# Performance work log

Measured on AMD Instinct MI355X. Metric: run time of the kernel, lower is better.

The kernel has to match this reference:

```python
import jax, jax.numpy as jnp
import numpy as np

DIMS = 96
HEADS = 2
E = 2.66
HID = int(DIMS * E)  # 255
B, H, W = 2, 256, 256
EPS = 1e-5


def setup_inputs() -> dict:
    key = jax.random.key(0)
    ks = jax.random.split(key, 8)
    s = 0.02
    return {
        "x": jax.random.normal(ks[0], (B, H, W, DIMS), jnp.float32),
        "ln1_gamma": jnp.ones((DIMS,), jnp.float32),
        "ln1_beta": jnp.zeros((DIMS,), jnp.float32),
        "ln2_gamma": jnp.ones((DIMS,), jnp.float32),
        "ln2_beta": jnp.zeros((DIMS,), jnp.float32),
        "qkv_w": jax.random.normal(ks[1], (DIMS, 3 * DIMS), jnp.float32) * s,
        "qkv_dw": jax.random.normal(ks[2], (3, 3, 3 * DIMS), jnp.float32) * s,
        "temperature": jnp.ones((HEADS, 1, 1), jnp.float32),
        "attn_out_w": jax.random.normal(ks[3], (DIMS, DIMS), jnp.float32) * s,
        "ffn_in_w": jax.random.normal(ks[4], (DIMS, 2 * HID), jnp.float32) * s,
        "ffn_dw": jax.random.normal(ks[5], (3, 3, 2 * HID), jnp.float32) * s,
        "ffn_out_w": jax.random.normal(ks[6], (HID, DIMS), jnp.float32) * s,
    }


def _layernorm(x, gamma, beta):
    # tf.nn.moments over channel axis (biased variance), per-pixel LN
    mu = jnp.mean(x, axis=-1, keepdims=True)
    var = jnp.var(x, axis=-1, keepdims=True)
    return (x - mu) / jnp.sqrt(var + EPS) * gamma + beta


def _dwconv3x3(x, k):
    # x: [B,H,W,C]; k: [3,3,C] depthwise kernel, SAME padding, no bias
    c = x.shape[-1]
    return jax.lax.conv_general_dilated(
        x, k[:, :, None, :], (1, 1), 'SAME',
        dimension_numbers=('NHWC', 'HWIO', 'NHWC'), feature_group_count=c)


def reference(x, ln1_gamma, ln1_beta, ln2_gamma, ln2_beta, qkv_w, qkv_dw,
              temperature, attn_out_w, ffn_in_w, ffn_dw, ffn_out_w):
    b, h, w, c = x.shape
    ch = c // HEADS  # per-head channels

    # ---- transposed (channel) attention branch ----
    y = _layernorm(x, ln1_gamma, ln1_beta)
    qkv = _dwconv3x3(jnp.einsum('bhwc,cd->bhwd', y, qkv_w), qkv_dw)
    q, k, v = jnp.split(qkv, 3, axis=-1)

    def to_heads(t):  # [b,h,w,heads*ch] -> [b,heads,ch,hw]
        return t.reshape(b, h * w, HEADS, ch).transpose(0, 2, 3, 1)

    q, k, v = to_heads(q), to_heads(k), to_heads(v)
    q = q / jnp.linalg.norm(q, axis=-1, keepdims=True)  # L2 over spatial dim
    k = k / jnp.linalg.norm(k, axis=-1, keepdims=True)
    # small [b,heads,ch,ch] attention matrix
    attn = jax.nn.softmax(jnp.einsum('bncs,bnds->bncd', q, k) * temperature, axis=-1)
    o = jnp.einsum('bncd,bnds->bncs', attn, v)  # [b,heads,ch,hw]
    o = o.transpose(0, 3, 1, 2).reshape(b, h, w, c)
    x = x + jnp.einsum('bhwc,cd->bhwd', o, attn_out_w)

    # ---- gated depthwise-conv FFN branch ----
    y = _layernorm(x, ln2_gamma, ln2_beta)
    hdd = _dwconv3x3(jnp.einsum('bhwc,cd->bhwd', y, ffn_in_w), ffn_dw)
    x1, x2 = jnp.split(hdd, 2, axis=-1)
    gated = jax.nn.gelu(x1, approximate=False) * x2  # tf.nn.gelu default = exact
    x = x + jnp.einsum('bhwc,cd->bhwd', gated, ffn_out_w)
    return x
```

## Files before the change

### kernel.cpp

```cpp
#include <hip/hip_runtime.h>
#include <hip/hip_bf16.h>

typedef __hip_bfloat16 bf16;
typedef __attribute__((ext_vector_type(8))) short short8;
typedef __attribute__((ext_vector_type(4))) float floatx4;

#define NPIX  131072
#define BATCH 2
#define HH    256
#define WW    256
#define CDIM  96
#define C3    288
#define HEADS 2
#define CH    48
#define HIDN  255
#define HWSZ  65536
#define EPSV  1e-5f

__device__ __forceinline__ float b2f(bf16 v) { return __bfloat162float(v); }
__device__ __forceinline__ bf16  f2b(float v) { return __float2bfloat16(v); }
__device__ __forceinline__ short f2bs(float v) { bf16 h = __float2bfloat16(v); return *reinterpret_cast<short*>(&h); }
__device__ __forceinline__ float lo16(unsigned u) { return __uint_as_float(u << 16); }
__device__ __forceinline__ float hi16(unsigned u) { return __uint_as_float(u & 0xffff0000u); }
__device__ __forceinline__ unsigned packbf(float lo, float hi) {
  return ((unsigned)(unsigned short)f2bs(hi) << 16) | (unsigned)(unsigned short)f2bs(lo);
}

__device__ __forceinline__ float fast_gelu(float x) {
  float ax = fabsf(x) * 0.70710678118654752440f;
  float t  = 1.f / (1.f + 0.3275911f * ax);
  float p  = ((((1.061405429f * t - 1.453152027f) * t + 1.421413741f) * t
               - 0.284496736f) * t + 0.254829592f) * t;
  float er = 1.f - p * __expf(-ax * ax);
  er = copysignf(er, x);
  return 0.5f * x * (1.f + er);
}

__global__ __launch_bounds__(256) void prep_wt(
    const float* __restrict__ qkv_w, const float* __restrict__ ffn_in_w,
    const float* __restrict__ ffn_out_w, const float* __restrict__ ffn_dw,
    bf16* __restrict__ WQ, bf16* __restrict__ WF1, bf16* __restrict__ WF2,
    bf16* __restrict__ WO, float* __restrict__ WDW)
{
  int gid = blockIdx.x * 256 + threadIdx.x;
  if (gid < 27648) {
    int n = gid / 96, k = gid - n * 96;
    WQ[gid] = f2b(qkv_w[k * C3 + n]);
  } else if (gid < 27648 + 24576) {
    int g = gid - 27648;
    int n = g / 96, k = g - n * 96;
    WF1[g] = f2b(n < HIDN ? ffn_in_w[k * (2 * HIDN) + n] : 0.f);
  } else if (gid < 27648 + 49152) {
    int g = gid - 27648 - 24576;
    int n = g / 96, k = g - n * 96;
    WF2[g] = f2b(n < HIDN ? ffn_in_w[k * (2 * HIDN) + HIDN + n] : 0.f);
  } else if (gid < 101376) {
    int g = gid - 27648 - 49152;
    int n = g / 256, k = g - n * 256;
    WO[g] = f2b(k < HIDN ? ffn_out_w[k * CDIM + n] : 0.f);
  } else {
    int idx = gid - 101376;
    if (idx < 4608) {
      int c = idx & 511;
      float v = 0.f;
      if (c < 255)                 v = ffn_dw[(idx >> 9) * 510 + c];
      else if (c >= 256 && c < 511) v = ffn_dw[(idx >> 9) * 510 + (c - 1)];
      WDW[idx] = v;
    }
  }
}

template<int BM, int BN, int KT, bool ADD_RES, bool OUT_BF16>
__global__ __launch_bounds__(256, 2) void mfma_gemm(
    const bf16* __restrict__ A, int lda,
    const bf16* __restrict__ Wt,
    void* __restrict__ outp, int ldo,
    const float* __restrict__ res, int ldr)
{
  constexpr int NK  = KT / 32;
  constexpr int NCT = BN / 16;
  constexpr int RT  = BM / 64;
  const int tid  = threadIdx.x;
  const long bm  = (long)blockIdx.x * BM;
  const int lane = tid & 63;
  const int wv   = tid >> 6;
  const int m15  = lane & 15;
  const int quad = lane >> 4;

  short8 areg[RT][NK];
  #pragma unroll
  for (int rt = 0; rt < RT; ++rt) {
    const bf16* ap = A + (bm + wv * (BM / 4) + rt * 16 + m15) * lda + quad * 8;
    #pragma unroll
    for (int kk = 0; kk < NK; ++kk)
      areg[rt][kk] = *reinterpret_cast<const short8*>(ap + kk * 32);
  }

  floatx4 acc[RT][NCT];
  #pragma unroll
  for (int rt = 0; rt < RT; ++rt)
    #pragma unroll
    for (int ct = 0; ct < NCT; ++ct)
      acc[rt][ct] = (floatx4){0.f, 0.f, 0.f, 0.f};

  const bf16* wp = Wt + m15 * KT + quad * 8;
  #pragma unroll
  for (int kk = 0; kk < NK; ++kk)
    #pragma unroll
    for (int ct = 0; ct < NCT; ++ct) {
      short8 b = *reinterpret_cast<const short8*>(wp + ct * 16 * KT + kk * 32);
      #pragma unroll
      for (int rt = 0; rt < RT; ++rt)
        acc[rt][ct] = __builtin_amdgcn_mfma_f32_16x16x32_bf16(areg[rt][kk], b, acc[rt][ct], 0, 0, 0);
    }

  #pragma unroll
  for (int rt = 0; rt < RT; ++rt)
    #pragma unroll
    for (int ct = 0; ct < NCT; ++ct) {
      int col = ct * 16 + m15;
      #pragma unroll
      for (int r = 0; r < 4; ++r) {
        long row = bm + wv * (BM / 4) + rt * 16 + quad * 4 + r;
        float v = acc[rt][ct][r];
        if (ADD_RES) v += res[row * ldr + col];
        if (OUT_BF16) ((bf16*)outp)[row * ldo + col] = f2b(v);
        else          ((float*)outp)[row * ldo + col] = v;
      }
    }
}

__global__ __launch_bounds__(256, 2) void mfma_gemm_ffn(
    const bf16* __restrict__ A,
    const bf16* __restrict__ Wt1, const bf16* __restrict__ Wt2,
    bf16* __restrict__ out1, bf16* __restrict__ out2)
{
  const bf16* Wt  = blockIdx.z ? Wt2 : Wt1;
  bf16* outp      = blockIdx.z ? out2 : out1;
  const int tid  = threadIdx.x;
  const long bm  = (long)blockIdx.x * 128;
  const int lane = tid & 63;
  const int wv   = tid >> 6;
  const int m15  = lane & 15;
  const int quad = lane >> 4;

  short8 areg[2][3];
  #pragma unroll
  for (int rt = 0; rt < 2; ++rt) {
    const bf16* ap = A + (bm + wv * 32 + rt * 16 + m15) * CDIM + quad * 8;
    #pragma unroll
    for (int kk = 0; kk < 3; ++kk)
      areg[rt][kk] = *reinterpret_cast<const short8*>(ap + kk * 32);
  }

  floatx4 acc[2][16];
  #pragma unroll
  for (int rt = 0; rt < 2; ++rt)
    #pragma unroll
    for (int ct = 0; ct < 16; ++ct)
      acc[rt][ct] = (floatx4){0.f, 0.f, 0.f, 0.f};

  const bf16* wp = Wt + m15 * 96 + quad * 8;
  #pragma unroll
  for (int kk = 0; kk < 3; ++kk)
    #pragma unroll
    for (int ct = 0; ct < 16; ++ct) {
      short8 b = *reinterpret_cast<const short8*>(wp + ct * 16 * 96 + kk * 32);
      #pragma unroll
      for (int rt = 0; rt < 2; ++rt)
        acc[rt][ct] = __builtin_amdgcn_mfma_f32_16x16x32_bf16(areg[rt][kk], b, acc[rt][ct], 0, 0, 0);
    }

  #pragma unroll
  for (int rt = 0; rt < 2; ++rt)
    #pragma unroll
    for (int ct = 0; ct < 16; ++ct) {
      int col = ct * 16 + m15;
      #pragma unroll
      for (int r = 0; r < 4; ++r) {
        long row = bm + wv * 32 + rt * 16 + quad * 4 + r;
        outp[row * 256 + col] = f2b(acc[rt][ct][r]);
      }
    }
}

__global__ __launch_bounds__(256, 2) void mfma_gemm_lnA(
    const float* __restrict__ X, const float* __restrict__ gam, const float* __restrict__ bet,
    const bf16* __restrict__ Wt,
    bf16* __restrict__ outp)
{
  const int tid  = threadIdx.x;
  const long bm  = (long)blockIdx.x * 128;
  const int lane = tid & 63;
  const int wv   = tid >> 6;
  const int m15  = lane & 15;
  const int quad = lane >> 4;

  float xv[2][24];
  #pragma unroll
  for (int rt = 0; rt < 2; ++rt) {
    const float* xp = X + (bm + wv * 32 + rt * 16 + m15) * CDIM + quad * 8;
    #pragma unroll
    for (int kk = 0; kk < 3; ++kk) {
      float4 t0 = *reinterpret_cast<const float4*>(xp + kk * 32);
      float4 t1 = *reinterpret_cast<const float4*>(xp + kk * 32 + 4);
      xv[rt][kk * 8 + 0] = t0.x; xv[rt][kk * 8 + 1] = t0.y; xv[rt][kk * 8 + 2] = t0.z; xv[rt][kk * 8 + 3] = t0.w;
      xv[rt][kk * 8 + 4] = t1.x; xv[rt][kk * 8 + 5] = t1.y; xv[rt][kk * 8 + 6] = t1.z; xv[rt][kk * 8 + 7] = t1.w;
    }
  }
  float gv[24], bv[24];
  #pragma unroll
  for (int kk = 0; kk < 3; ++kk) {
    float4 g0 = *reinterpret_cast<const float4*>(gam + kk * 32 + quad * 8);
    float4 g1 = *reinterpret_cast<const float4*>(gam + kk * 32 + quad * 8 + 4);
    float4 b0 = *reinterpret_cast<const float4*>(bet + kk * 32 + quad * 8);
    float4 b1 = *reinterpret_cast<const float4*>(bet + kk * 32 + quad * 8 + 4);
    gv[kk * 8 + 0] = g0.x; gv[kk * 8 + 1] = g0.y; gv[kk * 8 + 2] = g0.z; gv[kk * 8 + 3] = g0.w;
    gv[kk * 8 + 4] = g1.x; gv[kk * 8 + 5] = g1.y; gv[kk * 8 + 6] = g1.z; gv[kk * 8 + 7] = g1.w;
    bv[kk * 8 + 0] = b0.x; bv[kk * 8 + 1] = b0.y; bv[kk * 8 + 2] = b0.z; bv[kk * 8 + 3] = b0.w;
    bv[kk * 8 + 4] = b1.x; bv[kk * 8 + 5] = b1.y; bv[kk * 8 + 6] = b1.z; bv[kk * 8 + 7] = b1.w;
  }

  short8 areg[2][3];
  #pragma unroll
  for (int rt = 0; rt < 2; ++rt) {
    float s = 0.f, sq = 0.f;
    #pragma unroll
    for (int e = 0; e < 24; ++e) { s += xv[rt][e]; sq += xv[rt][e] * xv[rt][e]; }
    s  += __shfl_xor(s, 16);  s  += __shfl_xor(s, 32);
    sq += __shfl_xor(sq, 16); sq += __shfl_xor(sq, 32);
    float mean = s * (1.f / 96.f);
    float var  = sq * (1.f / 96.f) - mean * mean;
    float rstd = rsqrtf(var + EPSV);
    #pragma unroll
    for (int kk = 0; kk < 3; ++kk)
      #pragma unroll
      for (int j = 0; j < 8; ++j)
        areg[rt][kk][j] = f2bs((xv[rt][kk * 8 + j] - mean) * rstd * gv[kk * 8 + j] + bv[kk * 8 + j]);
  }

  floatx4 acc[2][18];
  #pragma unroll
  for (int rt = 0; rt < 2; ++rt)
    #pragma unroll
    for (int ct = 0; ct < 18; ++ct)
      acc[rt][ct] = (floatx4){0.f, 0.f, 0.f, 0.f};

  const bf16* wp = Wt + m15 * 96 + quad * 8;
  #pragma unroll
  for (int kk = 0; kk < 3; ++kk)
    #pragma unroll
    for (int ct = 0; ct < 18; ++ct) {
      short8 b = *reinterpret_cast<const short8*>(wp + ct * 16 * 96 + kk * 32);
      #pragma unroll
      for (int rt = 0; rt < 2; ++rt)
        acc[rt][ct] = __builtin_amdgcn_mfma_f32_16x16x32_bf16(areg[rt][kk], b, acc[rt][ct], 0, 0, 0);
    }

  #pragma unroll
  for (int rt = 0; rt < 2; ++rt)
    #pragma unroll
    for (int ct = 0; ct < 18; ++ct) {
      int col = ct * 16 + m15;
      #pragma unroll
      for (int r = 0; r < 4; ++r) {
        long row = bm + wv * 32 + rt * 16 + quad * 4 + r;
        outp[row * C3 + col] = f2b(acc[rt][ct][r]);
      }
    }
}

__global__ __launch_bounds__(256, 2) void mfma_gemm_attn(
    const bf16* __restrict__ A, const bf16* __restrict__ Mt,
    const float* __restrict__ res, const float* __restrict__ gam, const float* __restrict__ bet,
    float* __restrict__ outp, bf16* __restrict__ y2)
{
  const int tid  = threadIdx.x;
  const long bm  = (long)blockIdx.x * 128;
  const int lane = tid & 63;
  const int wv   = tid >> 6;
  const int m15  = lane & 15;
  const int quad = lane >> 4;

  short8 areg[2][3];
  #pragma unroll
  for (int rt = 0; rt < 2; ++rt) {
    const bf16* ap = A + (bm + wv * 32 + rt * 16 + m15) * 96 + quad * 8;
    #pragma unroll
    for (int kk = 0; kk < 3; ++kk)
      areg[rt][kk] = *reinterpret_cast<const short8*>(ap + kk * 32);
  }

  floatx4 acc[2][6];
  #pragma unroll
  for (int rt = 0; rt < 2; ++rt)
    #pragma unroll
    for (int ct = 0; ct < 6; ++ct)
      acc[rt][ct] = (floatx4){0.f, 0.f, 0.f, 0.f};

  const bf16* mp = Mt + (bm >> 16) * (CDIM * CDIM) + m15 * 96 + quad * 8;
  #pragma unroll
  for (int kk = 0; kk < 3; ++kk)
    #pragma unroll
    for (int ct = 0; ct < 6; ++ct) {
      short8 b = *reinterpret_cast<const short8*>(mp + ct * 16 * 96 + kk * 32);
      #pragma unroll
      for (int rt = 0; rt < 2; ++rt)
        acc[rt][ct] = __builtin_amdgcn_mfma_f32_16x16x32_bf16(areg[rt][kk], b, acc[rt][ct], 0, 0, 0);
    }

  float gv[6], bv[6];
  #pragma unroll
  for (int ct = 0; ct < 6; ++ct) { gv[ct] = gam[ct * 16 + m15]; bv[ct] = bet[ct * 16 + m15]; }

  #pragma unroll
  for (int rt = 0; rt < 2; ++rt)
    #pragma unroll
    for (int r = 0; r < 4; ++r) {
      long row = bm + wv * 32 + rt * 16 + quad * 4 + r;
      float v[6];
      float s = 0.f, sq = 0.f;
      #pragma unroll
      for (int ct = 0; ct < 6; ++ct) {
        v[ct] = acc[rt][ct][r] + res[row * CDIM + ct * 16 + m15];
        s += v[ct]; sq += v[ct] * v[ct];
      }
      #pragma unroll
      for (int off = 8; off; off >>= 1) { s += __shfl_xor(s, off); sq += __shfl_xor(sq, off); }
      float mean = s * (1.f / 96.f);
      float var  = sq * (1.f / 96.f) - mean * mean;
      float rstd = rsqrtf(var + EPSV);
      #pragma unroll
      for (int ct = 0; ct < 6; ++ct) {
        int col = ct * 16 + m15;
        outp[row * CDIM + col] = v[ct];
        y2[row * CDIM + col] = f2b((v[ct] - mean) * rstd * gv[ct] + bv[ct]);
      }
    }
}

__global__ __launch_bounds__(384, 2) void dwconv_plane(
    const bf16* __restrict__ in,
    const float* __restrict__ kw,
    bf16* __restrict__ outbase)
{
  __shared__ uint4 sm[12][19 * 10];
  const int tid = threadIdx.x;
  const int tx0 = blockIdx.x * 16;
  const int ty0 = (blockIdx.y & 31) * 8;
  const int b   = blockIdx.y >> 5;
  const int pl  = blockIdx.z;
  const int c0  = pl * 96;
  const long bbase = (long)b * HWSZ;
  bf16* out = outbase + (size_t)pl * NPIX * 96;

  const int lane = tid & 63;
  const int wv   = tid >> 6;

  for (int f = lane; f < 180; f += 64) {
    int row = f / 18, px = f - row * 18;
    int y = ty0 + row - 1, xx = tx0 + px - 1;
    uint4 ua = make_uint4(0u, 0u, 0u, 0u), ub = ua;
    if ((unsigned)y < (unsigned)HH && (unsigned)xx < (unsigned)WW) {
      const bf16* p = in + (bbase + (long)y * WW + xx) * C3 + c0;
      ua = *reinterpret_cast<const uint4*>(p + wv * 8);
      ub = *reinterpret_cast<const uint4*>(p + (wv + 6) * 8);
    }
    sm[wv][row * 19 + px]     = ua;
    sm[wv + 6][row * 19 + px] = ub;
  }
  asm volatile("s_waitcnt lgkmcnt(0)" ::: "memory");
  __builtin_amdgcn_sched_barrier(0);

  const int x  = lane & 15;
  const int yg = lane >> 4;

  #pragma unroll 1
  for (int cgi = 0; cgi < 2; ++cgi) {
    const int cg = wv + cgi * 6;
    const int cbu = __builtin_amdgcn_readfirstlane(c0 + cg * 8);
    float wgt[9][8];
    #pragma unroll
    for (int t = 0; t < 9; ++t) {
      float4 w0 = *reinterpret_cast<const float4*>(kw + t * C3 + cbu);
      float4 w1 = *reinterpret_cast<const float4*>(kw + t * C3 + cbu + 4);
      wgt[t][0] = w0.x; wgt[t][1] = w0.y; wgt[t][2] = w0.z; wgt[t][3] = w0.w;
      wgt[t][4] = w1.x; wgt[t][5] = w1.y; wgt[t][6] = w1.z; wgt[t][7] = w1.w;
    }
    #pragma unroll
    for (int yy = 0; yy < 2; ++yy) {
      const int ry = yg * 2 + yy;
      float acc[8] = {0.f, 0.f, 0.f, 0.f, 0.f, 0.f, 0.f, 0.f};
      #pragma unroll
      for (int dy = 0; dy < 3; ++dy)
        #pragma unroll
        for (int dx = 0; dx < 3; ++dx) {
          uint4 u = sm[cg][(ry + dy) * 19 + x + dx];
          const float* wt = wgt[dy * 3 + dx];
          acc[0] += lo16(u.x) * wt[0]; acc[1] += hi16(u.x) * wt[1];
          acc[2] += lo16(u.y) * wt[2]; acc[3] += hi16(u.y) * wt[3];
          acc[4] += lo16(u.z) * wt[4]; acc[5] += hi16(u.z) * wt[5];
          acc[6] += lo16(u.w) * wt[6]; acc[7] += hi16(u.w) * wt[7];
        }
      bf16* op = out + (bbase + (long)(ty0 + ry) * WW + tx0 + x) * 96 + cg * 8;
      __align__(16) bf16 ov[8];
      #pragma unroll
      for (int j = 0; j < 8; ++j) ov[j] = f2b(acc[j]);
      *reinterpret_cast<uint4*>(op) = *reinterpret_cast<const uint4*>(ov);
    }
    __builtin_amdgcn_sched_barrier(0);
  }
}

__global__ __launch_bounds__(512, 2) void dwgate512(
    const bf16* __restrict__ t1, const bf16* __restrict__ t2,
    const float* __restrict__ wdw, bf16* __restrict__ out)
{
  __shared__ uint4 sm[8][19 * 10];
  const int tid = threadIdx.x;
  const int tx0 = blockIdx.x * 16;
  const int ty0 = (blockIdx.y & 31) * 8;
  const long bbase = (long)(blockIdx.y >> 5) * HWSZ;
  const int c0  = blockIdx.z * 64;

  const int lane = tid & 63;
  const int wv   = tid >> 6;
  const int cb   = c0 + wv * 8;
  const int cbu  = __builtin_amdgcn_readfirstlane(cb);

  uint4 t2r[3];
  #pragma unroll
  for (int i = 0; i < 3; ++i) {
    int f = lane + i * 64;
    int row = f / 18, px = f - row * 18;
    int y = ty0 + row - 1, xx = tx0 + px - 1;
    bool ok = (f < 180) && ((unsigned)y < (unsigned)HH) && ((unsigned)xx < (unsigned)WW);
    long base = (bbase + (long)y * WW + xx) * 256 + cb;
    uint4 u1 = make_uint4(0u, 0u, 0u, 0u);
    t2r[i]   = make_uint4(0u, 0u, 0u, 0u);
    if (ok) {
      u1     = *reinterpret_cast<const uint4*>(t1 + base);
      t2r[i] = *reinterpret_cast<const uint4*>(t2 + base);
    }
    if (f < 180) sm[wv][row * 19 + px] = u1;
  }
  asm volatile("s_waitcnt lgkmcnt(0)" ::: "memory");
  __builtin_amdgcn_sched_barrier(0);

  const int x  = lane & 15;
  const int yg = lane >> 4;

  unsigned gp[8];
  float wgt[9][8];

  #pragma unroll
  for (int t = 0; t < 9; ++t) {
    float4 w0 = *reinterpret_cast<const float4*>(wdw + t * 512 + cbu);
    float4 w1 = *reinterpret_cast<const float4*>(wdw + t * 512 + cbu + 4);
    wgt[t][0] = w0.x; wgt[t][1] = w0.y; wgt[t][2] = w0.z; wgt[t][3] = w0.w;
    wgt[t][4] = w1.x; wgt[t][5] = w1.y; wgt[t][6] = w1.z; wgt[t][7] = w1.w;
  }
  #pragma unroll
  for (int yy = 0; yy < 2; ++yy) {
    const int ry = yg * 2 + yy;
    float acc[8] = {0.f, 0.f, 0.f, 0.f, 0.f, 0.f, 0.f, 0.f};
    #pragma unroll
    for (int dy = 0; dy < 3; ++dy)
      #pragma unroll
      for (int dx = 0; dx < 3; ++dx) {
        uint4 u = sm[wv][(ry + dy) * 19 + x + dx];
        const float* wt = wgt[dy * 3 + dx];
        acc[0] += lo16(u.x) * wt[0]; acc[1] += hi16(u.x) * wt[1];
        acc[2] += lo16(u.y) * wt[2]; acc[3] += hi16(u.y) * wt[3];
        acc[4] += lo16(u.z) * wt[4]; acc[5] += hi16(u.z) * wt[5];
        acc[6] += lo16(u.w) * wt[6]; acc[7] += hi16(u.w) * wt[7];
      }
    #pragma unroll
    for (int p = 0; p < 4; ++p)
      gp[yy * 4 + p] = packbf(fast_gelu(acc[2 * p]), fast_gelu(acc[2 * p + 1]));
  }

  asm volatile("s_waitcnt lgkmcnt(0)" ::: "memory");
  __builtin_amdgcn_sched_barrier(0);
  #pragma unroll
  for (int i = 0; i < 3; ++i) {
    int f = lane + i * 64;
    int row = f / 18, px = f - row * 18;
    if (f < 180) sm[wv][row * 19 + px] = t2r[i];
  }
  asm volatile("s_waitcnt lgkmcnt(0)" ::: "memory");
  __builtin_amdgcn_sched_barrier(0);

  #pragma unroll
  for (int t = 0; t < 9; ++t) {
    float4 w0 = *reinterpret_cast<const float4*>(wdw + t * 512 + 256 + cbu);
    float4 w1 = *reinterpret_cast<const float4*>(wdw + t * 512 + 256 + cbu + 4);
    wgt[t][0] = w0.x; wgt[t][1] = w0.y; wgt[t][2] = w0.z; wgt[t][3] = w0.w;
    wgt[t][4] = w1.x; wgt[t][5] = w1.y; wgt[t][6] = w1.z; wgt[t][7] = w1.w;
  }
  #pragma unroll
  for (int yy = 0; yy < 2; ++yy) {
    const int ry = yg * 2 + yy;
    float acc[8] = {0.f, 0.f, 0.f, 0.f, 0.f, 0.f, 0.f, 0.f};
    #pragma unroll
    for (int dy = 0; dy < 3; ++dy)
      #pragma unroll
      for (int dx = 0; dx < 3; ++dx) {
        uint4 u = sm[wv][(ry + dy) * 19 + x + dx];
        const float* wt = wgt[dy * 3 + dx];
        acc[0] += lo16(u.x) * wt[0]; acc[1] += hi16(u.x) * wt[1];
        acc[2] += lo16(u.y) * wt[2]; acc[3] += hi16(u.y) * wt[3];
        acc[4] += lo16(u.z) * wt[4]; acc[5] += hi16(u.z) * wt[5];
        acc[6] += lo16(u.w) * wt[6]; acc[7] += hi16(u.w) * wt[7];
      }
    bf16* op = out + (bbase + (long)(ty0 + ry) * WW + tx0 + x) * 256 + cb;
    __align__(16) bf16 ov[8];
    #pragma unroll
    for (int p = 0; p < 4; ++p) {
      ov[2 * p]     = f2b(lo16(gp[yy * 4 + p]) * acc[2 * p]);
      ov[2 * p + 1] = f2b(hi16(gp[yy * 4 + p]) * acc[2 * p + 1]);
    }
    *reinterpret_cast<uint4*>(op) = *reinterpret_cast<const uint4*>(ov);
  }
}

__global__ __launch_bounds__(256) void gram_kernel(
    const bf16* __restrict__ Qp, const bf16* __restrict__ Kp,
    float* __restrict__ Gpart, float* __restrict__ Npart)
{
  constexpr int SP = 264;
  __shared__ __align__(16) char raw[2 * CH * SP * 2];
  short* qs = (short*)raw;
  short* ks = qs + CH * SP;
  const int tid  = threadIdx.x;
  const int bh   = blockIdx.y;
  const long row0 = (long)(bh >> 1) * HWSZ + (long)blockIdx.x * 256;
  const int head = bh & 1;
  const int lane = tid & 63;
  const int wv   = tid >> 6;
  const int m15  = lane & 15;
  const int quad = lane >> 4;

  {
    const short* qsrc = (const short*)(Qp + (row0 + tid) * 96 + head * CH);
    const short* ksrc = (const short*)(Kp + (row0 + tid) * 96 + head * CH);
    #pragma unroll
    for (int v = 0; v < 6; ++v) {
      short8 q8 = *reinterpret_cast<const short8*>(qsrc + v * 8);
      short8 k8 = *reinterpret_cast<const short8*>(ksrc + v * 8);
      #pragma unroll
      for (int j = 0; j < 8; ++j) {
        qs[(v * 8 + j) * SP + tid] = q8[j];
        ks[(v * 8 + j) * SP + tid] = k8[j];
      }
    }
  }
  __syncthreads();

  floatx4 acc[3][3], accq[3], acck[3];
  #pragma unroll
  for (int i = 0; i < 3; ++i) {
    accq[i] = (floatx4){0.f, 0.f, 0.f, 0.f};
    acck[i] = (floatx4){0.f, 0.f, 0.f, 0.f};
    #pragma unroll
    for (int j = 0; j < 3; ++j) acc[i][j] = (floatx4){0.f, 0.f, 0.f, 0.f};
  }

  #pragma unroll
  for (int kk = 0; kk < 2; ++kk) {
    const int s_off = wv * 64 + kk * 32 + quad * 8;
    short8 aq[3], bk[3];
    #pragma unroll
    for (int i = 0; i < 3; ++i) {
      aq[i] = *reinterpret_cast<const short8*>(&qs[(i * 16 + m15) * SP + s_off]);
      bk[i] = *reinterpret_cast<const short8*>(&ks[(i * 16 + m15) * SP + s_off]);
    }
    #pragma unroll
    for (int i = 0; i < 3; ++i) {
      accq[i] = __builtin_amdgcn_mfma_f32_16x16x32_bf16(aq[i], aq[i], accq[i], 0, 0, 0);
      acck[i] = __builtin_amdgcn_mfma_f32_16x16x32_bf16(bk[i], bk[i], acck[i], 0, 0, 0);
      #pragma unroll
      for (int j = 0; j < 3; ++j)
        acc[i][j] = __builtin_amdgcn_mfma_f32_16x16x32_bf16(aq[i], bk[j], acc[i][j], 0, 0, 0);
    }
  }

  __syncthreads();
  float* part  = (float*)raw;
  float* npart = part + 4 * 48 * 49;
  const int c_lo = quad * 4;
  #pragma unroll
  for (int i = 0; i < 3; ++i)
    #pragma unroll
    for (int j = 0; j < 3; ++j)
      #pragma unroll
      for (int r = 0; r < 4; ++r)
        part[wv * 2352 + (i * 16 + c_lo + r) * 49 + j * 16 + m15] = acc[i][j][r];
  if (m15 >= c_lo && m15 < c_lo + 4) {
    const int r = m15 - c_lo;
    #pragma unroll
    for (int i = 0; i < 3; ++i) {
      npart[wv * 96 + i * 16 + m15]      = accq[i][r];
      npart[wv * 96 + 48 + i * 16 + m15] = acck[i][r];
    }
  }
  __syncthreads();
  float* Gp = Gpart + ((long)blockIdx.x * 4 + bh) * 2304;
  for (int f = tid; f < 2304; f += 256) {
    int row = f / 48, col = f - row * 48;
    int o = row * 49 + col;
    Gp[f] = part[o] + part[2352 + o] + part[4704 + o] + part[7056 + o];
  }
  if (tid < 96)
    Npart[((long)blockIdx.x * 4 + bh) * 96 + tid] =
        npart[tid] + npart[96 + tid] + npart[192 + tid] + npart[288 + tid];
}

__global__ __launch_bounds__(256) void gram_reduce(const float* __restrict__ Gpart,
    const float* __restrict__ Npart, float* __restrict__ G,
    float* __restrict__ nq, float* __restrict__ nk)
{
  const int bh = blockIdx.x;
  const int b = bh >> 1, head = bh & 1;
  if (blockIdx.y < 9) {
    const int f = blockIdx.y * 256 + threadIdx.x;
    float s = 0.f;
    #pragma unroll 8
    for (int c = 0; c < 256; ++c) s += Gpart[((long)c * 4 + bh) * 2304 + f];
    G[(long)bh * 2304 + f] = s;
  } else {
    const int t = threadIdx.x;
    if (t < 96) {
      float s = 0.f;
      #pragma unroll 8
      for (int c = 0; c < 256; ++c) s += Npart[((long)c * 4 + bh) * 96 + t];
      if (t < 48) nq[b * CDIM + head * CH + t] = s;
      else        nk[b * CDIM + head * CH + t - 48] = s;
    }
  }
}

__global__ __launch_bounds__(64) void softmax_kernel(const float* __restrict__ G,
    const float* __restrict__ nq, const float* __restrict__ nk,
    const float* __restrict__ temp, float* __restrict__ attn)
{
  int r = blockIdx.x;
  int lane = threadIdx.x;
  int bh = r / CH, c = r % CH;
  int b = bh >> 1, head = bh & 1;
  float t  = temp[head];
  float qn = sqrtf(nq[b * CDIM + head * CH + c]);
  float val = 0.f, v = -INFINITY;
  if (lane < CH) {
    float kn = sqrtf(nk[b * CDIM + head * CH + lane]);
    val = G[r * CH + lane] / (qn * kn) * t;
    v = val;
  }
  float m = v;
  #pragma unroll
  for (int off = 32; off; off >>= 1) m = fmaxf(m, __shfl_xor(m, off));
  float e = (lane < CH) ? expf(val - m) : 0.f;
  float s = e;
  #pragma unroll
  for (int off = 32; off; off >>= 1) s += __shfl_xor(s, off);
  if (lane < CH) attn[r * CH + lane] = e / s;
}

__global__ __launch_bounds__(256) void attnmat_kernel(const float* __restrict__ attn,
    const float* __restrict__ aow, bf16* __restrict__ Mt)
{
  const int b  = blockIdx.x;
  const int k0 = blockIdx.y * 16;
  for (int idx = threadIdx.x; idx < 16 * 96; idx += 256) {
    int k = k0 + idx / 96, n = idx % 96;
    int h = k / CH, kk = k % CH;
    const float* ap = attn + ((b * 2 + h) * CH) * CH + kk;
    const float* wp = aow + (h * CH) * CDIM + n;
    float acc = 0.f;
    #pragma unroll
    for (int cc = 0; cc < CH; ++cc) acc += ap[cc * CH] * wp[cc * CDIM];
    Mt[(long)b * CDIM * CDIM + n * CDIM + k] = f2b(acc);
  }
}

extern "C" void kernel_launch(void* const* d_in, const int* in_sizes, int n_in,
                              void* d_out, int out_size, void* d_ws, size_t ws_size,
                              hipStream_t stream)
{
  const float* x          = (const float*)d_in[0];
  const float* ln1_g      = (const float*)d_in[1];
  const float* ln1_b      = (const float*)d_in[2];
  const float* ln2_g      = (const float*)d_in[3];
  const float* ln2_b      = (const float*)d_in[4];
  const float* qkv_w      = (const float*)d_in[5];
  const float* qkv_dw     = (const float*)d_in[6];
  const float* temp       = (const float*)d_in[7];
  const float* attn_out_w = (const float*)d_in[8];
  const float* ffn_in_w   = (const float*)d_in[9];
  const float* ffn_dw     = (const float*)d_in[10];
  const float* ffn_out_w  = (const float*)d_in[11];
  float* out = (float*)d_out;

  char* ws = (char*)d_ws;
  size_t off = 0;
  auto alloc = [&](size_t bytes) { void* p = ws + off; off += (bytes + 255) & ~(size_t)255; return p; };
  bf16*  BA  = (bf16*)alloc((size_t)NPIX * C3 * 2);
  bf16*  BB  = (bf16*)alloc((size_t)NPIX * C3 * 2);
  bf16*  BC  = (bf16*)alloc((size_t)NPIX * CDIM * 2);
  float* NQ  = (float*)alloc(BATCH * CDIM * 4);
  float* NK  = (float*)alloc(BATCH * CDIM * 4);
  float* G   = (float*)alloc(BATCH * HEADS * CH * CH * 4);
  float* ATT = (float*)alloc(BATCH * HEADS * CH * CH * 4);
  bf16*  MT  = (bf16*)alloc((size_t)BATCH * CDIM * CDIM * 2);
  bf16*  WQ  = (bf16*)alloc(288 * 96 * 2);
  bf16*  WF1 = (bf16*)alloc(256 * 96 * 2);
  bf16*  WF2 = (bf16*)alloc(256 * 96 * 2);
  bf16*  WO  = (bf16*)alloc(96 * 256 * 2);
  float* WDW = (float*)alloc(9 * 512 * 4);
  bf16*  T2M = (bf16*)alloc((size_t)NPIX * 256 * 2);
  const bool merged = (off <= ws_size);

  bf16* Qp = BA;
  bf16* Kp = BA + (size_t)NPIX * 96;
  bf16* Vp = BA + (size_t)2 * NPIX * 96;

  float* GP = (float*)BB;
  float* NP = GP + (size_t)256 * 4 * 2304;

  prep_wt<<<414, 256, 0, stream>>>(qkv_w, ffn_in_w, ffn_out_w, ffn_dw,
                                   WQ, WF1, WF2, WO, WDW);

  mfma_gemm_lnA<<<NPIX / 128, 256, 0, stream>>>(x, ln1_g, ln1_b, WQ, BB);
  dwconv_plane<<<dim3(16, 64, 3), 384, 0, stream>>>(BB, qkv_dw, BA);
  gram_kernel<<<dim3(256, 4), 256, 0, stream>>>(Qp, Kp, GP, NP);
  gram_reduce<<<dim3(4, 10), 256, 0, stream>>>(GP, NP, G, NQ, NK);
  softmax_kernel<<<192, 64, 0, stream>>>(G, NQ, NK, temp, ATT);
  attnmat_kernel<<<dim3(2, 6), 256, 0, stream>>>(ATT, attn_out_w, MT);
  mfma_gemm_attn<<<NPIX / 128, 256, 0, stream>>>(
      Vp, MT, x, ln2_g, ln2_b, out, BC);

  if (merged) {
    mfma_gemm_ffn<<<dim3(NPIX / 128, 1, 2), 256, 0, stream>>>(BC, WF1, WF2, BA, T2M);
    dwgate512<<<dim3(16, 64, 4), 512, 0, stream>>>(BA, T2M, WDW, BB);
  } else {
    for (int b = 0; b < BATCH; ++b) {
      const bf16* bc = BC + (size_t)b * HWSZ * CDIM;
      bf16* t1    = BA;
      bf16* t2    = BA + (size_t)HWSZ * 256;
      bf16* gated = BB + (size_t)b * HWSZ * 256;
      mfma_gemm_ffn<<<dim3(HWSZ / 128, 1, 2), 256, 0, stream>>>(bc, WF1, WF2, t1, t2);
      dwgate512<<<dim3(16, 32, 4), 512, 0, stream>>>(t1, t2, WDW, gated);
    }
  }
  mfma_gemm<128, 96, 256, true, false><<<NPIX / 128, 256, 0, stream>>>(
      BB, 256, WO, out, CDIM, out, CDIM);
}
```

Measured before the change: 450.6 us.

## Swap MFMA operands so each lane writes packed 8-byte output rows

The LN+QKV and FFN-in GEMM kernels now pass the weights as the A operand and the pixel fragment as B. The accumulator's four values then sit along consecutive output channels of a single pixel, so each lane packs them into one 8-byte bf16 store instead of four scattered 2-byte stores. Each wave now covers 16 pixels instead of 32, so blocks handle 64 pixels and the grid doubles. This trades weight-fragment reuse across two row tiles for coalesced, vectorized stores and lower register pressure.

```diff
diff --git a/kernel.cpp b/kernel.cpp
--- a/kernel.cpp
+++ b/kernel.cpp
@@ -138,50 +138,39 @@
   const bf16* Wt  = blockIdx.z ? Wt2 : Wt1;
   bf16* outp      = blockIdx.z ? out2 : out1;
   const int tid  = threadIdx.x;
-  const long bm  = (long)blockIdx.x * 128;
   const int lane = tid & 63;
   const int wv   = tid >> 6;
   const int m15  = lane & 15;
   const int quad = lane >> 4;
-
-  short8 areg[2][3];
-  #pragma unroll
-  for (int rt = 0; rt < 2; ++rt) {
-    const bf16* ap = A + (bm + wv * 32 + rt * 16 + m15) * CDIM + quad * 8;
-    #pragma unroll
-    for (int kk = 0; kk < 3; ++kk)
-      areg[rt][kk] = *reinterpret_cast<const short8*>(ap + kk * 32);
-  }
-
-  floatx4 acc[2][16];
-  #pragma unroll
-  for (int rt = 0; rt < 2; ++rt)
-    #pragma unroll
-    for (int ct = 0; ct < 16; ++ct)
-      acc[rt][ct] = (floatx4){0.f, 0.f, 0.f, 0.f};
+  const long pix = (long)blockIdx.x * 64 + wv * 16 + m15;
+
+  short8 pfrag[3];
+  const bf16* ap = A + pix * CDIM + quad * 8;
+  #pragma unroll
+  for (int kk = 0; kk < 3; ++kk)
+    pfrag[kk] = *reinterpret_cast<const short8*>(ap + kk * 32);
+
+  floatx4 acc[16];
+  #pragma unroll
+  for (int ct = 0; ct < 16; ++ct) acc[ct] = (floatx4){0.f, 0.f, 0.f, 0.f};
 
   const bf16* wp = Wt + m15 * 96 + quad * 8;
   #pragma unroll
   for (int kk = 0; kk < 3; ++kk)
     #pragma unroll
     for (int ct = 0; ct < 16; ++ct) {
-      short8 b = *reinterpret_cast<const short8*>(wp + ct * 16 * 96 + kk * 32);
-      #pragma unroll
-      for (int rt = 0; rt < 2; ++rt)
-        acc[rt][ct] = __builtin_amdgcn_mfma_f32_16x16x32_bf16(areg[rt][kk], b, acc[rt][ct], 0, 0, 0);
-    }
-
-  #pragma unroll
-  for (int rt = 0; rt < 2; ++rt)
-    #pragma unroll
-    for (int ct = 0; ct < 16; ++ct) {
-      int col = ct * 16 + m15;
-      #pragma unroll
-      for (int r = 0; r < 4; ++r) {
-        long row = bm + wv * 32 + rt * 16 + quad * 4 + r;
-        outp[row * 256 + col] = f2b(acc[rt][ct][r]);
-      }
-    }
+      short8 w = *reinterpret_cast<const short8*>(wp + ct * 16 * 96 + kk * 32);
+      acc[ct] = __builtin_amdgcn_mfma_f32_16x16x32_bf16(w, pfrag[kk], acc[ct], 0, 0, 0);
+    }
+
+  bf16* op = outp + pix * 256 + quad * 4;
+  #pragma unroll
+  for (int ct = 0; ct < 16; ++ct) {
+    uint2 pk;
+    pk.x = packbf(acc[ct][0], acc[ct][1]);
+    pk.y = packbf(acc[ct][2], acc[ct][3]);
+    *reinterpret_cast<uint2*>(op + ct * 16) = pk;
+  }
 }
 
 __global__ __launch_bounds__(256, 2) void mfma_gemm_lnA(
@@ -190,22 +179,21 @@
     bf16* __restrict__ outp)
 {
   const int tid  = threadIdx.x;
-  const long bm  = (long)blockIdx.x * 128;
   const int lane = tid & 63;
   const int wv   = tid >> 6;
   const int m15  = lane & 15;
   const int quad = lane >> 4;
-
-  float xv[2][24];
-  #pragma unroll
-  for (int rt = 0; rt < 2; ++rt) {
-    const float* xp = X + (bm + wv * 32 + rt * 16 + m15) * CDIM + quad * 8;
+  const long pix = (long)blockIdx.x * 64 + wv * 16 + m15;
+
+  float xv[24];
+  {
+    const float* xp = X + pix * CDIM + quad * 8;
     #pragma unroll
     for (int kk = 0; kk < 3; ++kk) {
       float4 t0 = *reinterpret_cast<const float4*>(xp + kk * 32);
       float4 t1 = *reinterpret_cast<const float4*>(xp + kk * 32 + 4);
-      xv[rt][kk * 8 + 0] = t0.x; xv[rt][kk * 8 + 1] = t0.y; xv[rt][kk * 8 + 2] = t0.z; xv[rt][kk * 8 + 3] = t0.w;
-      xv[rt][kk * 8 + 4] = t1.x; xv[rt][kk * 8 + 5] = t1.y; xv[rt][kk * 8 + 6] = t1.z; xv[rt][kk * 8 + 7] = t1.w;
+      xv[kk * 8 + 0] = t0.x; xv[kk * 8 + 1] = t0.y; xv[kk * 8 + 2] = t0.z; xv[kk * 8 + 3] = t0.w;
+      xv[kk * 8 + 4] = t1.x; xv[kk * 8 + 5] = t1.y; xv[kk * 8 + 6] = t1.z; xv[kk * 8 + 7] = t1.w;
     }
   }
   float gv[24], bv[24];
@@ -221,53 +209,43 @@
     bv[kk * 8 + 4] = b1.x; bv[kk * 8 + 5] = b1.y; bv[kk * 8 + 6] = b1.z; bv[kk * 8 + 7] = b1.w;
   }
 
-  short8 areg[2][3];
-  #pragma unroll
-  for (int rt = 0; rt < 2; ++rt) {
-    float s = 0.f, sq = 0.f;
-    #pragma unroll
-    for (int e = 0; e < 24; ++e) { s += xv[rt][e]; sq += xv[rt][e] * xv[rt][e]; }
-    s  += __shfl_xor(s, 16);  s  += __shfl_xor(s, 32);
-    sq += __shfl_xor(sq, 16); sq += __shfl_xor(sq, 32);
-    float mean = s * (1.f / 96.f);
-    float var  = sq * (1.f / 96.f) - mean * mean;
-    float rstd = rsqrtf(var + EPSV);
-    #pragma unroll
-    for (int kk = 0; kk < 3; ++kk)
-      #pragma unroll
-      for (int j = 0; j < 8; ++j)
-        areg[rt][kk][j] = f2bs((xv[rt][kk * 8 + j] - mean) * rstd * gv[kk * 8 + j] + bv[kk * 8 + j]);
-  }
-
-  floatx4 acc[2][18];
-  #pragma unroll
-  for (int rt = 0; rt < 2; ++rt)
-    #pragma unroll
-    for (int ct = 0; ct < 18; ++ct)
-      acc[rt][ct] = (floatx4){0.f, 0.f, 0.f, 0.f};
+  float s = 0.f, sq = 0.f;
+  #pragma unroll
+  for (int e = 0; e < 24; ++e) { s += xv[e]; sq += xv[e] * xv[e]; }
+  s  += __shfl_xor(s, 16);  s  += __shfl_xor(s, 32);
+  sq += __shfl_xor(sq, 16); sq += __shfl_xor(sq, 32);
+  float mean = s * (1.f / 96.f);
+  float var  = sq * (1.f / 96.f) - mean * mean;
+  float rstd = rsqrtf(var + EPSV);
+
+  short8 areg[3];
+  #pragma unroll
+  for (int kk = 0; kk < 3; ++kk)
+    #pragma unroll
+    for (int j = 0; j < 8; ++j)
+      areg[kk][j] = f2bs((xv[kk * 8 + j] - mean) * rstd * gv[kk * 8 + j] + bv[kk * 8 + j]);
+
+  floatx4 acc[18];
+  #pragma unroll
+  for (int ct = 0; ct < 18; ++ct) acc[ct] = (floatx4){0.f, 0.f, 0.f, 0.f};
 
   const bf16* wp = Wt + m15 * 96 + quad * 8;
   #pragma unroll
   for (int kk = 0; kk < 3; ++kk)
     #pragma unroll
     for (int ct = 0; ct < 18; ++ct) {
-      short8 b = *reinterpret_cast<const short8*>(wp + ct * 16 * 96 + kk * 32);
-      #pragma unroll
-      for (int rt = 0; rt < 2; ++rt)
-        acc[rt][ct] = __builtin_amdgcn_mfma_f32_16x16x32_bf16(areg[rt][kk], b, acc[rt][ct], 0, 0, 0);
-    }
-
-  #pragma unroll
-  for (int rt = 0; rt < 2; ++rt)
-    #pragma unroll
-    for (int ct = 0; ct < 18; ++ct) {
-      int col = ct * 16 + m15;
-      #pragma unroll
-      for (int r = 0; r < 4; ++r) {
-        long row = bm + wv * 32 + rt * 16 + quad * 4 + r;
-        outp[row * C3 + col] = f2b(acc[rt][ct][r]);
-      }
-    }
+      short8 w = *reinterpret_cast<const short8*>(wp + ct * 16 * 96 + kk * 32);
+      acc[ct] = __builtin_amdgcn_mfma_f32_16x16x32_bf16(w, areg[kk], acc[ct], 0, 0, 0);
+    }
+
+  bf16* op = outp + pix * C3 + quad * 4;
+  #pragma unroll
+  for (int ct = 0; ct < 18; ++ct) {
+    uint2 pk;
+    pk.x = packbf(acc[ct][0], acc[ct][1]);
+    pk.y = packbf(acc[ct][2], acc[ct][3]);
+    *reinterpret_cast<uint2*>(op + ct * 16) = pk;
+  }
 }
 
 __global__ __launch_bounds__(256, 2) void mfma_gemm_attn(
@@ -730,7 +708,7 @@
   prep_wt<<<414, 256, 0, stream>>>(qkv_w, ffn_in_w, ffn_out_w, ffn_dw,
                                    WQ, WF1, WF2, WO, WDW);
 
-  mfma_gemm_lnA<<<NPIX / 128, 256, 0, stream>>>(x, ln1_g, ln1_b, WQ, BB);
+  mfma_gemm_lnA<<<NPIX / 64, 256, 0, stream>>>(x, ln1_g, ln1_b, WQ, BB);
   dwconv_plane<<<dim3(16, 64, 3), 384, 0, stream>>>(BB, qkv_dw, BA);
   gram_kernel<<<dim3(256, 4), 256, 0, stream>>>(Qp, Kp, GP, NP);
   gram_reduce<<<dim3(4, 10), 256, 0, stream>>>(GP, NP, G, NQ, NK);
@@ -740,7 +718,7 @@
       Vp, MT, x, ln2_g, ln2_b, out, BC);
 
   if (merged) {
-    mfma_gemm_ffn<<<dim3(NPIX / 128, 1, 2), 256, 0, stream>>>(BC, WF1, WF2, BA, T2M);
+    mfma_gemm_ffn<<<dim3(NPIX / 64, 1, 2), 256, 0, stream>>>(BC, WF1, WF2, BA, T2M);
     dwgate512<<<dim3(16, 64, 4), 512, 0, stream>>>(BA, T2M, WDW, BB);
   } else {
     for (int b = 0; b < BATCH; ++b) {
@@ -748,7 +726,7 @@
       bf16* t1    = BA;
       bf16* t2    = BA + (size_t)HWSZ * 256;
       bf16* gated = BB + (size_t)b * HWSZ * 256;
-      mfma_gemm_ffn<<<dim3(HWSZ / 128, 1, 2), 256, 0, stream>>>(bc, WF1, WF2, t1, t2);
+      mfma_gemm_ffn<<<dim3(HWSZ / 64, 1, 2), 256, 0, stream>>>(bc, WF1, WF2, t1, t2);
       dwgate512<<<dim3(16, 32, 4), 512, 0, stream>>>(t1, t2, WDW, gated);
     }
   }
```

After: 480.8 us. +6.7%, slower.
